# Kernel tuning notes

Measured on AMD Instinct MI355X. Metric: run time of the kernel, lower is better.

## Reference

```python
import jax, jax.numpy as jnp
import numpy as np

RADIUS = 0.5
K = 32
EPS = 1e-5


def ball_query(pc, new_pc, radius, k):
    """pc [B,3,N], new_pc [B,3,S] -> idx [B,S,k] int32, num [B,S] int32.
    First k in-radius points per query; empty slots filled with the first
    found index (standard ball-query semantics of QueryDepthPoint)."""
    d2 = jnp.sum((new_pc[:, :, :, None] - pc[:, :, None, :]) ** 2, axis=1)  # [B,S,N]
    B, S, N = d2.shape
    mask = d2 < radius * radius
    rank = jnp.cumsum(mask.astype(jnp.int32), axis=-1) - 1          # rank among valid
    slot = jnp.where(mask & (rank < k), rank, k)                     # k = dummy slot
    jidx = jnp.broadcast_to(jnp.arange(N, dtype=jnp.int32), (B, S, N))
    bidx = jnp.arange(B)[:, None, None]
    sidx = jnp.arange(S)[None, :, None]
    idx = jnp.zeros((B, S, k + 1), jnp.int32).at[bidx, sidx, slot].set(jidx)
    idx = idx[..., :k]
    num = jnp.sum(mask, axis=-1).astype(jnp.int32)                   # [B,S]
    nvalid = jnp.minimum(num, k)
    idx = jnp.where(jnp.arange(k) < nvalid[..., None], idx, idx[..., :1])
    return idx, num


def conv_bn_relu(x, w, b, g, be):
    """1x1 Conv2d + BatchNorm2d (batch stats, training mode) + ReLU.
    x [B,Cin,S,K], w [Cout,Cin]."""
    y = jnp.einsum('bcsk,oc->bosk', x, w) + b[None, :, None, None]
    mean = jnp.mean(y, axis=(0, 2, 3), keepdims=True)
    var = jnp.var(y, axis=(0, 2, 3), keepdims=True)
    y = (y - mean) * jax.lax.rsqrt(var + EPS) * g[None, :, None, None] + be[None, :, None, None]
    return jax.nn.relu(y)


def setup_inputs() -> dict:
    key = jax.random.key(0)
    ks = jax.random.split(key, 8)
    B, N, S, C = 4, 8192, 2048, 16
    mlp = [32, 32, 64]
    cin = C + 3  # use_xyz concat
    pc = jax.random.normal(ks[0], (B, 3, N), jnp.float32)
    feat = jax.random.normal(ks[1], (B, C, N), jnp.float32)
    new_pc = jax.random.normal(ks[2], (B, 3, S), jnp.float32)
    def kaiming(k, co, ci):
        return jax.random.normal(k, (co, ci), jnp.float32) * np.sqrt(2.0 / ci)
    w1 = kaiming(ks[3], mlp[0], cin)
    w2 = kaiming(ks[4], mlp[1], mlp[0])
    w3 = kaiming(ks[5], mlp[2], mlp[1])
    return {
        'pc': pc, 'feat': feat, 'new_pc': new_pc,
        'w1': w1, 'b1': jnp.zeros((mlp[0],)), 'g1': jnp.ones((mlp[0],)), 'be1': jnp.zeros((mlp[0],)),
        'w2': w2, 'b2': jnp.zeros((mlp[1],)), 'g2': jnp.ones((mlp[1],)), 'be2': jnp.zeros((mlp[1],)),
        'w3': w3, 'b3': jnp.zeros((mlp[2],)), 'g3': jnp.ones((mlp[2],)), 'be3': jnp.zeros((mlp[2],)),
    }


def reference(pc, feat, new_pc, w1, b1, g1, be1, w2, b2, g2, be2, w3, b3, g3, be3):
    B = pc.shape[0]
    S = new_pc.shape[2]
    idx, num = ball_query(pc, new_pc, RADIUS, K)          # [B,S,K], [B,S]
    bidx = jnp.arange(B)[:, None, None]
    # gather neighbors: fancy index -> [B,S,K,3] / [B,S,K,Cf], then to channel-first
    grouped_pc = pc[bidx, :, idx].transpose(0, 3, 1, 2)   # [B,3,S,K]
    grouped_pc = grouped_pc - new_pc[:, :, :, None]       # center on query
    grouped_feat = feat[bidx, :, idx].transpose(0, 3, 1, 2)  # [B,Cf,S,K]
    x = jnp.concatenate([grouped_pc, grouped_feat], axis=1)  # [B,Cf+3,S,K]
    x = conv_bn_relu(x, w1, b1, g1, be1)
    x = conv_bn_relu(x, w2, b2, g2, be2)
    x = conv_bn_relu(x, w3, b3, g3, be3)
    valid = (num > 0).astype(x.dtype)[:, None, :, None]   # [B,1,S,1]
    return x * valid
```

## Files before the change

### kernel.cpp

```cpp
#include <hip/hip_runtime.h>

#define BQ_RADIUS2 0.25f
#define KK 32
#define NB 4
#define NP 8192
#define NS 2048
#define C1 32
#define C2 32
#define C3 64
#define EPSBN 1e-5f
#define RTOT 65536
#define MTOT (NB*NS*KK)
#define NSLOT 32

#define OFF_G     0
#define OFF_IDX   655360
#define OFF_VALID 917504
#define OFF_P1    925696
#define OFF_P2    927744
#define OFF_P3    929792
#define OFF_PAR1  933888
#define OFF_PAR2  933952
#define OFF_PAR3  934016

__global__ __launch_bounds__(256) void k_pack(const float* __restrict__ pc,
                                              const float* __restrict__ feat,
                                              float* __restrict__ g,
                                              float* __restrict__ partials) {
  const int t = blockIdx.x * 256 + threadIdx.x;
  if (t < 8192) partials[t] = 0.f;
  const int b = t >> 13;
  const int j = t & (NP - 1);
  const float* pcb = pc + b * 3 * NP;
  float* gp = g + (size_t)t * 20;
  gp[0] = pcb[j];
  gp[1] = pcb[NP + j];
  gp[2] = pcb[2 * NP + j];
  const float* fb = feat + b * 16 * NP;
#pragma unroll
  for (int c = 0; c < 16; c++) gp[3 + c] = fb[c * NP + j];
  gp[19] = 0.f;
}

__global__ __launch_bounds__(256) void k_ballquery(const float* __restrict__ pc,
                                                   const float* __restrict__ newpc,
                                                   int* __restrict__ idx,
                                                   int* __restrict__ valid) {
  __shared__ int buf[4][KK];
  const int tid = threadIdx.x;
  const int w = tid >> 6, lane = tid & 63;
  const int gq = blockIdx.x * 4 + w;
  const int b = gq >> 11, s = gq & (NS - 1);
  const float* np0 = newpc + b * 3 * NS;
  const float qx = np0[s], qy = np0[NS + s], qz = np0[2 * NS + s];
  const float* px = pc + b * 3 * NP;
  const float* py = px + NP;
  const float* pz = px + 2 * NP;
  if (lane == 0) buf[w][0] = 0;
  int cnt = 0;
  for (int j0 = 0; j0 < NP; j0 += 256) {
    const int jb = j0 + lane * 4;
    const float4 vx = *(const float4*)(px + jb);
    const float4 vy = *(const float4*)(py + jb);
    const float4 vz = *(const float4*)(pz + jb);
    int mm = 0;
    {
      float dx = __fsub_rn(qx, vx.x), dy = __fsub_rn(qy, vy.x), dz = __fsub_rn(qz, vz.x);
      if (__fadd_rn(__fadd_rn(__fmul_rn(dx, dx), __fmul_rn(dy, dy)), __fmul_rn(dz, dz)) < BQ_RADIUS2) mm |= 1;
    }
    {
      float dx = __fsub_rn(qx, vx.y), dy = __fsub_rn(qy, vy.y), dz = __fsub_rn(qz, vz.y);
      if (__fadd_rn(__fadd_rn(__fmul_rn(dx, dx), __fmul_rn(dy, dy)), __fmul_rn(dz, dz)) < BQ_RADIUS2) mm |= 2;
    }
    {
      float dx = __fsub_rn(qx, vx.z), dy = __fsub_rn(qy, vy.z), dz = __fsub_rn(qz, vz.z);
      if (__fadd_rn(__fadd_rn(__fmul_rn(dx, dx), __fmul_rn(dy, dy)), __fmul_rn(dz, dz)) < BQ_RADIUS2) mm |= 4;
    }
    {
      float dx = __fsub_rn(qx, vx.w), dy = __fsub_rn(qy, vy.w), dz = __fsub_rn(qz, vz.w);
      if (__fadd_rn(__fadd_rn(__fmul_rn(dx, dx), __fmul_rn(dy, dy)), __fmul_rn(dz, dz)) < BQ_RADIUS2) mm |= 8;
    }
    const int c4 = __popc(mm);
    int pre = c4;
#pragma unroll
    for (int off = 1; off < 64; off <<= 1) {
      int v = __shfl_up(pre, off);
      if (lane >= off) pre += v;
    }
    const int total = __shfl(pre, 63);
    if (mm) {
      int base = cnt + pre - c4;
#pragma unroll
      for (int i = 0; i < 4; i++) {
        if ((mm >> i) & 1) {
          if (base < KK) buf[w][base] = jb + i;
          base++;
        }
      }
    }
    cnt += total;
    if (cnt >= KK) break;
  }
  __syncthreads();
  if (lane < KK) {
    const int f = cnt < KK ? cnt : KK;
    const int i0 = buf[w][0];
    idx[gq * KK + lane] = (lane < f) ? buf[w][lane] : i0;
  }
  if (lane == 0) valid[gq] = (cnt > 0);
}

__global__ __launch_bounds__(256, 1) void k_conv1(const float* __restrict__ g,
                                                  const int* __restrict__ idx,
                                                  const float* __restrict__ newpc,
                                                  const float* __restrict__ w1,
                                                  const float* __restrict__ b1,
                                                  float* __restrict__ y,
                                                  float* __restrict__ partial) {
  __shared__ float wl[C1 * 20];
  __shared__ float bl[C1];
  __shared__ float red[16][2 * C1 + 1];
  const int tid = threadIdx.x;
  for (int i = tid; i < C1 * 20; i += 256) {
    const int o = i / 20, c = i - o * 20;
    wl[i] = (c < 19) ? w1[o * 19 + c] : 0.f;
  }
  if (tid < C1) bl[tid] = b1[tid];
  __syncthreads();
  const int pos = blockIdx.x * 256 + tid;
  const int p4 = pos << 2;
  const int b = p4 >> 16;
  const int r = p4 & (RTOT - 1);
  const int s = r >> 5;
  const int4 jj = *(const int4*)(idx + p4);
  const float* np0 = newpc + b * 3 * NS;
  const float nx = np0[s], ny = np0[NS + s], nz = np0[2 * NS + s];
  float4 xr[20];
#define LOADPT(COMP, J) { \
    const float4* gp = (const float4*)(g + (size_t)(b * NP + (J)) * 20); \
    const float4 a0 = gp[0], a1 = gp[1], a2 = gp[2], a3 = gp[3], a4 = gp[4]; \
    xr[0].COMP = a0.x - nx; xr[1].COMP = a0.y - ny; xr[2].COMP = a0.z - nz; xr[3].COMP = a0.w; \
    xr[4].COMP = a1.x; xr[5].COMP = a1.y; xr[6].COMP = a1.z; xr[7].COMP = a1.w; \
    xr[8].COMP = a2.x; xr[9].COMP = a2.y; xr[10].COMP = a2.z; xr[11].COMP = a2.w; \
    xr[12].COMP = a3.x; xr[13].COMP = a3.y; xr[14].COMP = a3.z; xr[15].COMP = a3.w; \
    xr[16].COMP = a4.x; xr[17].COMP = a4.y; xr[18].COMP = a4.z; xr[19].COMP = a4.w; }
  LOADPT(x, jj.x) LOADPT(y, jj.y) LOADPT(z, jj.z) LOADPT(w, jj.w)
#undef LOADPT
  float* yb = y + ((size_t)b * C3) * RTOT + r;
  const int grp = tid >> 4;
  const bool lead = (tid & 15) == 0;
#pragma unroll 4
  for (int o = 0; o < C1; o++) {
    const float bo = bl[o];
    float4 acc = make_float4(bo, bo, bo, bo);
    const float4* wr = (const float4*)&wl[o * 20];
#pragma unroll
    for (int ct = 0; ct < 5; ct++) {
      const float4 wv = wr[ct];
      const float4 x0 = xr[4 * ct + 0], x1 = xr[4 * ct + 1], x2 = xr[4 * ct + 2], x3 = xr[4 * ct + 3];
      acc.x = fmaf(wv.x, x0.x, acc.x); acc.y = fmaf(wv.x, x0.y, acc.y);
      acc.z = fmaf(wv.x, x0.z, acc.z); acc.w = fmaf(wv.x, x0.w, acc.w);
      acc.x = fmaf(wv.y, x1.x, acc.x); acc.y = fmaf(wv.y, x1.y, acc.y);
      acc.z = fmaf(wv.y, x1.z, acc.z); acc.w = fmaf(wv.y, x1.w, acc.w);
      acc.x = fmaf(wv.z, x2.x, acc.x); acc.y = fmaf(wv.z, x2.y, acc.y);
      acc.z = fmaf(wv.z, x2.z, acc.z); acc.w = fmaf(wv.z, x2.w, acc.w);
      acc.x = fmaf(wv.w, x3.x, acc.x); acc.y = fmaf(wv.w, x3.y, acc.y);
      acc.z = fmaf(wv.w, x3.z, acc.z); acc.w = fmaf(wv.w, x3.w, acc.w);
    }
    *(float4*)(yb + (size_t)o * RTOT) = acc;
    float a = (acc.x + acc.y) + (acc.z + acc.w);
    float q = (acc.x * acc.x + acc.y * acc.y) + (acc.z * acc.z + acc.w * acc.w);
    a += __shfl_xor(a, 1); q += __shfl_xor(q, 1);
    a += __shfl_xor(a, 2); q += __shfl_xor(q, 2);
    a += __shfl_xor(a, 4); q += __shfl_xor(q, 4);
    a += __shfl_xor(a, 8); q += __shfl_xor(q, 8);
    if (lead) { red[grp][o] = a; red[grp][C1 + o] = q; }
  }
  __syncthreads();
  if (tid < 2 * C1) {
    float v = 0.f;
#pragma unroll
    for (int gq = 0; gq < 16; gq++) v += red[gq][tid];
    atomicAdd(&partial[(blockIdx.x & (NSLOT - 1)) * 2 * C1 + tid], v);
  }
}

__global__ __launch_bounds__(256, 1) void k_conv2(const float* __restrict__ w2,
                                                  const float* __restrict__ b2,
                                                  const float* __restrict__ par,
                                                  float* y,
                                                  float* __restrict__ partial) {
  __shared__ float wl[C2 * C1];
  __shared__ float bl[C2];
  __shared__ float pl[2 * C1];
  __shared__ float red[16][2 * C2 + 1];
  const int tid = threadIdx.x;
  for (int i = tid; i < C2 * C1; i += 256) wl[i] = w2[i];
  if (tid < C2) bl[tid] = b2[tid];
  if (tid < 2 * C1) pl[tid] = par[tid];
  __syncthreads();
  const int pos = blockIdx.x * 256 + tid;
  const int p4 = pos << 2;
  const int b = p4 >> 16;
  const int r = p4 & (RTOT - 1);
  float* yb = y + ((size_t)b * C3) * RTOT + r;
  float4 xr[C1];
#pragma unroll
  for (int c = 0; c < C1; c++) {
    float4 v = *(const float4*)(yb + (size_t)c * RTOT);
    const float sc = pl[c], sh = pl[C1 + c];
    v.x = fmaxf(fmaf(v.x, sc, sh), 0.f);
    v.y = fmaxf(fmaf(v.y, sc, sh), 0.f);
    v.z = fmaxf(fmaf(v.z, sc, sh), 0.f);
    v.w = fmaxf(fmaf(v.w, sc, sh), 0.f);
    xr[c] = v;
  }
  const int grp = tid >> 4;
  const bool lead = (tid & 15) == 0;
#pragma unroll 4
  for (int o = 0; o < C2; o++) {
    const float bo = bl[o];
    float4 acc = make_float4(bo, bo, bo, bo);
    const float4* wr = (const float4*)&wl[o * C1];
#pragma unroll
    for (int ct = 0; ct < C1 / 4; ct++) {
      const float4 wv = wr[ct];
      const float4 x0 = xr[4 * ct + 0], x1 = xr[4 * ct + 1], x2 = xr[4 * ct + 2], x3 = xr[4 * ct + 3];
      acc.x = fmaf(wv.x, x0.x, acc.x); acc.y = fmaf(wv.x, x0.y, acc.y);
      acc.z = fmaf(wv.x, x0.z, acc.z); acc.w = fmaf(wv.x, x0.w, acc.w);
      acc.x = fmaf(wv.y, x1.x, acc.x); acc.y = fmaf(wv.y, x1.y, acc.y);
      acc.z = fmaf(wv.y, x1.z, acc.z); acc.w = fmaf(wv.y, x1.w, acc.w);
      acc.x = fmaf(wv.z, x2.x, acc.x); acc.y = fmaf(wv.z, x2.y, acc.y);
      acc.z = fmaf(wv.z, x2.z, acc.z); acc.w = fmaf(wv.z, x2.w, acc.w);
      acc.x = fmaf(wv.w, x3.x, acc.x); acc.y = fmaf(wv.w, x3.y, acc.y);
      acc.z = fmaf(wv.w, x3.z, acc.z); acc.w = fmaf(wv.w, x3.w, acc.w);
    }
    *(float4*)(yb + (size_t)o * RTOT) = acc;
    float a = (acc.x + acc.y) + (acc.z + acc.w);
    float q = (acc.x * acc.x + acc.y * acc.y) + (acc.z * acc.z + acc.w * acc.w);
    a += __shfl_xor(a, 1); q += __shfl_xor(q, 1);
    a += __shfl_xor(a, 2); q += __shfl_xor(q, 2);
    a += __shfl_xor(a, 4); q += __shfl_xor(q, 4);
    a += __shfl_xor(a, 8); q += __shfl_xor(q, 8);
    if (lead) { red[grp][o] = a; red[grp][C2 + o] = q; }
  }
  __syncthreads();
  if (tid < 2 * C2) {
    float v = 0.f;
#pragma unroll
    for (int gq = 0; gq < 16; gq++) v += red[gq][tid];
    atomicAdd(&partial[(blockIdx.x & (NSLOT - 1)) * 2 * C2 + tid], v);
  }
}

__global__ __launch_bounds__(256, 1) void k_conv3(const float* __restrict__ w3,
                                                  const float* __restrict__ b3,
                                                  const float* __restrict__ par,
                                                  float* y,
                                                  float* __restrict__ partial) {
  __shared__ float wl[C3 * C2];
  __shared__ float bl[C3];
  __shared__ float pl[2 * C2];
  __shared__ float red[16][2 * C3 + 1];
  const int tid = threadIdx.x;
  for (int i = tid; i < C3 * C2; i += 256) wl[i] = w3[i];
  if (tid < C3) bl[tid] = b3[tid];
  if (tid < 2 * C2) pl[tid] = par[tid];
  __syncthreads();
  const int pos = blockIdx.x * 256 + tid;
  const int p4 = pos << 2;
  const int b = p4 >> 16;
  const int r = p4 & (RTOT - 1);
  float* yb = y + ((size_t)b * C3) * RTOT + r;
  float4 xr[C2];
#pragma unroll
  for (int c = 0; c < C2; c++) {
    float4 v = *(const float4*)(yb + (size_t)c * RTOT);
    const float sc = pl[c], sh = pl[C2 + c];
    v.x = fmaxf(fmaf(v.x, sc, sh), 0.f);
    v.y = fmaxf(fmaf(v.y, sc, sh), 0.f);
    v.z = fmaxf(fmaf(v.z, sc, sh), 0.f);
    v.w = fmaxf(fmaf(v.w, sc, sh), 0.f);
    xr[c] = v;
  }
  const int grp = tid >> 4;
  const bool lead = (tid & 15) == 0;
#pragma unroll 4
  for (int o = 0; o < C3; o++) {
    const float bo = bl[o];
    float4 acc = make_float4(bo, bo, bo, bo);
    const float4* wr = (const float4*)&wl[o * C2];
#pragma unroll
    for (int ct = 0; ct < C2 / 4; ct++) {
      const float4 wv = wr[ct];
      const float4 x0 = xr[4 * ct + 0], x1 = xr[4 * ct + 1], x2 = xr[4 * ct + 2], x3 = xr[4 * ct + 3];
      acc.x = fmaf(wv.x, x0.x, acc.x); acc.y = fmaf(wv.x, x0.y, acc.y);
      acc.z = fmaf(wv.x, x0.z, acc.z); acc.w = fmaf(wv.x, x0.w, acc.w);
      acc.x = fmaf(wv.y, x1.x, acc.x); acc.y = fmaf(wv.y, x1.y, acc.y);
      acc.z = fmaf(wv.y, x1.z, acc.z); acc.w = fmaf(wv.y, x1.w, acc.w);
      acc.x = fmaf(wv.z, x2.x, acc.x); acc.y = fmaf(wv.z, x2.y, acc.y);
      acc.z = fmaf(wv.z, x2.z, acc.z); acc.w = fmaf(wv.z, x2.w, acc.w);
      acc.x = fmaf(wv.w, x3.x, acc.x); acc.y = fmaf(wv.w, x3.y, acc.y);
      acc.z = fmaf(wv.w, x3.z, acc.z); acc.w = fmaf(wv.w, x3.w, acc.w);
    }
    *(float4*)(yb + (size_t)o * RTOT) = acc;
    float a = (acc.x + acc.y) + (acc.z + acc.w);
    float q = (acc.x * acc.x + acc.y * acc.y) + (acc.z * acc.z + acc.w * acc.w);
    a += __shfl_xor(a, 1); q += __shfl_xor(q, 1);
    a += __shfl_xor(a, 2); q += __shfl_xor(q, 2);
    a += __shfl_xor(a, 4); q += __shfl_xor(q, 4);
    a += __shfl_xor(a, 8); q += __shfl_xor(q, 8);
    if (lead) { red[grp][o] = a; red[grp][C3 + o] = q; }
  }
  __syncthreads();
  if (tid < 2 * C3) {
    float v = 0.f;
#pragma unroll
    for (int gq = 0; gq < 16; gq++) v += red[gq][tid];
    atomicAdd(&partial[(blockIdx.x & (NSLOT - 1)) * 2 * C3 + tid], v);
  }
}

__global__ void k_params(const float* __restrict__ partial,
                         const float* __restrict__ gamma,
                         const float* __restrict__ beta,
                         float* __restrict__ params, int C) {
  __shared__ float tot[2 * C3];
  const int t = threadIdx.x;
  float v = 0.f;
#pragma unroll 1
  for (int sl = 0; sl < NSLOT; ++sl) v += partial[sl * 2 * C + t];
  tot[t] = v;
  __syncthreads();
  if (t < C) {
    const float inv = 1.0f / (float)MTOT;
    const float mean = tot[t] * inv;
    const float ex2 = tot[C + t] * inv;
    const float var = ex2 - mean * mean;
    const float sc = gamma[t] * rsqrtf(var + EPSBN);
    params[t] = sc;
    params[C + t] = beta[t] - mean * sc;
  }
}

__global__ __launch_bounds__(256) void k_final(float* __restrict__ out,
                                               const float* __restrict__ par,
                                               const int* __restrict__ valid) {
  const int t = blockIdx.x * 256 + threadIdx.x;
  const size_t e = (size_t)t * 4;
  const int b = t >> 20;
  const int o = (t >> 14) & 63;
  const int s = (t & 16383) >> 3;
  const float sc = par[o], sh = par[C3 + o];
  const float m = valid[(b << 11) + s] ? 1.f : 0.f;
  float4 v = *(float4*)(out + e);
  v.x = fmaxf(fmaf(v.x, sc, sh), 0.f) * m;
  v.y = fmaxf(fmaf(v.y, sc, sh), 0.f) * m;
  v.z = fmaxf(fmaf(v.z, sc, sh), 0.f) * m;
  v.w = fmaxf(fmaf(v.w, sc, sh), 0.f) * m;
  *(float4*)(out + e) = v;
}

extern "C" void kernel_launch(void* const* d_in, const int* in_sizes, int n_in,
                              void* d_out, int out_size, void* d_ws, size_t ws_size,
                              hipStream_t stream) {
  const float* pc    = (const float*)d_in[0];
  const float* feat  = (const float*)d_in[1];
  const float* newpc = (const float*)d_in[2];
  const float* w1 = (const float*)d_in[3];
  const float* b1 = (const float*)d_in[4];
  const float* g1 = (const float*)d_in[5];
  const float* be1 = (const float*)d_in[6];
  const float* w2 = (const float*)d_in[7];
  const float* b2 = (const float*)d_in[8];
  const float* g2 = (const float*)d_in[9];
  const float* be2 = (const float*)d_in[10];
  const float* w3 = (const float*)d_in[11];
  const float* b3 = (const float*)d_in[12];
  const float* g3 = (const float*)d_in[13];
  const float* be3 = (const float*)d_in[14];

  float* ws = (float*)d_ws;
  float* gbuf  = ws + OFF_G;
  int*   idx   = (int*)(ws + OFF_IDX);
  int*   valid = (int*)(ws + OFF_VALID);
  float* p1 = ws + OFF_P1;
  float* p2 = ws + OFF_P2;
  float* p3 = ws + OFF_P3;
  float* par1 = ws + OFF_PAR1;
  float* par2 = ws + OFF_PAR2;
  float* par3 = ws + OFF_PAR3;
  float* out = (float*)d_out;

  k_pack<<<dim3(128), dim3(256), 0, stream>>>(pc, feat, gbuf, p1);
  k_ballquery<<<dim3(2048), dim3(256), 0, stream>>>(pc, newpc, idx, valid);
  k_conv1<<<dim3(256), dim3(256), 0, stream>>>(gbuf, idx, newpc, w1, b1, out, p1);
  k_params<<<dim3(1), dim3(2 * C1), 0, stream>>>(p1, g1, be1, par1, C1);
  k_conv2<<<dim3(256), dim3(256), 0, stream>>>(w2, b2, par1, out, p2);
  k_params<<<dim3(1), dim3(2 * C2), 0, stream>>>(p2, g2, be2, par2, C2);
  k_conv3<<<dim3(256), dim3(256), 0, stream>>>(w3, b3, par2, out, p3);
  k_params<<<dim3(1), dim3(2 * C3), 0, stream>>>(p3, g3, be3, par3, C3);
  k_final<<<dim3(16384), dim3(256), 0, stream>>>(out, par3, valid);
}
```

Before: 245.5 us.

## Fuse conv/BN stages into one cooperative kernel with grid syncs

Replaces the three conv kernels, three BN parameter kernels and the final activation pass with a single cooperative kernel. Each thread keeps one gathered position's activations in registers across all three layers and uses grid-wide syncs to finalize batch-norm statistics between layers. This removes the intermediate round trips of activations through global memory and most launch overhead. In exchange it needs 1024 co-resident blocks of 256 threads with large per-thread register arrays, which risks spills or launch failure; if the cooperative launch fails, it falls back to the old multi-kernel path.

```diff
diff --git a/kernel.cpp b/kernel.cpp
--- a/kernel.cpp
+++ b/kernel.cpp
@@ -1,4 +1,7 @@
 #include <hip/hip_runtime.h>
+#include <hip/hip_cooperative_groups.h>
+
+namespace cg = cooperative_groups;
 
 #define BQ_RADIUS2 0.25f
 #define KK 32
@@ -110,7 +113,181 @@
   if (lane == 0) valid[gq] = (cnt > 0);
 }
 
-__global__ __launch_bounds__(256, 1) void k_conv1(const float* __restrict__ g,
+#define STAT_O(CC, O, ACC) { \
+    float a_ = (ACC), q_ = (ACC) * (ACC); \
+    a_ += __shfl_xor(a_, 1); q_ += __shfl_xor(q_, 1); \
+    a_ += __shfl_xor(a_, 2); q_ += __shfl_xor(q_, 2); \
+    a_ += __shfl_xor(a_, 4); q_ += __shfl_xor(q_, 4); \
+    a_ += __shfl_xor(a_, 8); q_ += __shfl_xor(q_, 8); \
+    if (lead) { red[grp][(O)] = a_; red[grp][(CC) + (O)] = q_; } }
+
+__global__ __launch_bounds__(256, 4) void k_mega(
+    const float* __restrict__ g, const int* __restrict__ idx,
+    const float* __restrict__ newpc, const int* __restrict__ valid,
+    const float* __restrict__ w1, const float* __restrict__ b1,
+    const float* __restrict__ g1, const float* __restrict__ be1,
+    const float* __restrict__ w2, const float* __restrict__ b2,
+    const float* __restrict__ g2, const float* __restrict__ be2,
+    const float* __restrict__ w3, const float* __restrict__ b3,
+    const float* __restrict__ g3, const float* __restrict__ be3,
+    float* __restrict__ out,
+    float* __restrict__ p1, float* __restrict__ p2, float* __restrict__ p3) {
+  cg::grid_group gridg = cg::this_grid();
+  __shared__ float red[16][2 * C3 + 1];
+  __shared__ float pl[2 * C3];
+  const int tid = threadIdx.x;
+  const int pos = blockIdx.x * 256 + tid;
+  const int b = pos >> 16;
+  const int r = pos & (RTOT - 1);
+  const int s = r >> 5;
+  const int grp = tid >> 4;
+  const bool lead = (tid & 15) == 0;
+  const int slot = blockIdx.x & (NSLOT - 1);
+
+  const int j = idx[pos];
+  const float4* gp = (const float4*)(g + (size_t)(b * NP + j) * 20);
+  const float4 a0 = gp[0], a1 = gp[1], a2 = gp[2], a3 = gp[3], a4 = gp[4];
+  const float* np0 = newpc + b * 3 * NS;
+  float xr[20];
+  xr[0] = a0.x - np0[s]; xr[1] = a0.y - np0[NS + s]; xr[2] = a0.z - np0[2 * NS + s]; xr[3] = a0.w;
+  xr[4] = a1.x; xr[5] = a1.y; xr[6] = a1.z; xr[7] = a1.w;
+  xr[8] = a2.x; xr[9] = a2.y; xr[10] = a2.z; xr[11] = a2.w;
+  xr[12] = a3.x; xr[13] = a3.y; xr[14] = a3.z; xr[15] = a3.w;
+  xr[16] = a4.x; xr[17] = a4.y; xr[18] = a4.z; xr[19] = a4.w;
+  float y1[C1];
+#pragma unroll 4
+  for (int o = 0; o < C1; o++) {
+    float acc = b1[o];
+    const float* wr = w1 + o * 19;
+#pragma unroll
+    for (int c = 0; c < 19; c++) acc = fmaf(wr[c], xr[c], acc);
+    y1[o] = acc;
+    STAT_O(C1, o, acc)
+  }
+  __syncthreads();
+  if (tid < 2 * C1) {
+    float v = 0.f;
+#pragma unroll
+    for (int gq = 0; gq < 16; gq++) v += red[gq][tid];
+    atomicAdd(&p1[slot * 2 * C1 + tid], v);
+  }
+  gridg.sync();
+  if (tid < C1) {
+    float sm = 0.f, sq = 0.f;
+#pragma unroll 1
+    for (int sl = 0; sl < NSLOT; sl++) {
+      sm += p1[sl * 2 * C1 + tid];
+      sq += p1[sl * 2 * C1 + C1 + tid];
+    }
+    const float inv = 1.f / (float)MTOT;
+    const float mean = sm * inv;
+    const float var = sq * inv - mean * mean;
+    const float sc = g1[tid] * rsqrtf(var + EPSBN);
+    pl[tid] = sc;
+    pl[C1 + tid] = be1[tid] - mean * sc;
+  }
+  __syncthreads();
+
+  float y2[C2];
+  {
+    float xn[C1];
+#pragma unroll
+    for (int c = 0; c < C1; c++) xn[c] = fmaxf(fmaf(y1[c], pl[c], pl[C1 + c]), 0.f);
+#pragma unroll 4
+    for (int o = 0; o < C2; o++) {
+      float acc = b2[o];
+      const float4* wr = (const float4*)(w2 + o * C1);
+#pragma unroll
+      for (int ct = 0; ct < C1 / 4; ct++) {
+        const float4 wv = wr[ct];
+        acc = fmaf(wv.x, xn[4 * ct + 0], acc);
+        acc = fmaf(wv.y, xn[4 * ct + 1], acc);
+        acc = fmaf(wv.z, xn[4 * ct + 2], acc);
+        acc = fmaf(wv.w, xn[4 * ct + 3], acc);
+      }
+      y2[o] = acc;
+      STAT_O(C2, o, acc)
+    }
+  }
+  __syncthreads();
+  if (tid < 2 * C2) {
+    float v = 0.f;
+#pragma unroll
+    for (int gq = 0; gq < 16; gq++) v += red[gq][tid];
+    atomicAdd(&p2[slot * 2 * C2 + tid], v);
+  }
+  gridg.sync();
+  if (tid < C2) {
+    float sm = 0.f, sq = 0.f;
+#pragma unroll 1
+    for (int sl = 0; sl < NSLOT; sl++) {
+      sm += p2[sl * 2 * C2 + tid];
+      sq += p2[sl * 2 * C2 + C2 + tid];
+    }
+    const float inv = 1.f / (float)MTOT;
+    const float mean = sm * inv;
+    const float var = sq * inv - mean * mean;
+    const float sc = g2[tid] * rsqrtf(var + EPSBN);
+    pl[tid] = sc;
+    pl[C2 + tid] = be2[tid] - mean * sc;
+  }
+  __syncthreads();
+
+  float y3[C3];
+  {
+    float xn[C2];
+#pragma unroll
+    for (int c = 0; c < C2; c++) xn[c] = fmaxf(fmaf(y2[c], pl[c], pl[C2 + c]), 0.f);
+#pragma unroll 4
+    for (int o = 0; o < C3; o++) {
+      float acc = b3[o];
+      const float4* wr = (const float4*)(w3 + o * C2);
+#pragma unroll
+      for (int ct = 0; ct < C2 / 4; ct++) {
+        const float4 wv = wr[ct];
+        acc = fmaf(wv.x, xn[4 * ct + 0], acc);
+        acc = fmaf(wv.y, xn[4 * ct + 1], acc);
+        acc = fmaf(wv.z, xn[4 * ct + 2], acc);
+        acc = fmaf(wv.w, xn[4 * ct + 3], acc);
+      }
+      y3[o] = acc;
+      STAT_O(C3, o, acc)
+    }
+  }
+  __syncthreads();
+  if (tid < 2 * C3) {
+    float v = 0.f;
+#pragma unroll
+    for (int gq = 0; gq < 16; gq++) v += red[gq][tid];
+    atomicAdd(&p3[slot * 2 * C3 + tid], v);
+  }
+  gridg.sync();
+  if (tid < C3) {
+    float sm = 0.f, sq = 0.f;
+#pragma unroll 1
+    for (int sl = 0; sl < NSLOT; sl++) {
+      sm += p3[sl * 2 * C3 + tid];
+      sq += p3[sl * 2 * C3 + C3 + tid];
+    }
+    const float inv = 1.f / (float)MTOT;
+    const float mean = sm * inv;
+    const float var = sq * inv - mean * mean;
+    const float sc = g3[tid] * rsqrtf(var + EPSBN);
+    pl[tid] = sc;
+    pl[C3 + tid] = be3[tid] - mean * sc;
+  }
+  __syncthreads();
+
+  const float m = valid[(b << 11) + s] ? 1.f : 0.f;
+  float* ob = out + ((size_t)b * C3) * RTOT + r;
+#pragma unroll 8
+  for (int o = 0; o < C3; o++) {
+    ob[(size_t)o * RTOT] = fmaxf(fmaf(y3[o], pl[o], pl[C3 + o]), 0.f) * m;
+  }
+}
+
+
+__global__ __launch_bounds__(256, 1) void f_conv1(const float* __restrict__ g,
                                                   const int* __restrict__ idx,
                                                   const float* __restrict__ newpc,
                                                   const float* __restrict__ w1,
@@ -185,7 +362,7 @@
   }
 }
 
-__global__ __launch_bounds__(256, 1) void k_conv2(const float* __restrict__ w2,
+__global__ __launch_bounds__(256, 1) void f_conv2(const float* __restrict__ w2,
                                                   const float* __restrict__ b2,
                                                   const float* __restrict__ par,
                                                   float* y,
@@ -253,7 +430,7 @@
   }
 }
 
-__global__ __launch_bounds__(256, 1) void k_conv3(const float* __restrict__ w3,
+__global__ __launch_bounds__(256, 1) void f_conv3(const float* __restrict__ w3,
                                                   const float* __restrict__ b3,
                                                   const float* __restrict__ par,
                                                   float* y,
@@ -321,7 +498,7 @@
   }
 }
 
-__global__ void k_params(const float* __restrict__ partial,
+__global__ void f_params(const float* __restrict__ partial,
                          const float* __restrict__ gamma,
                          const float* __restrict__ beta,
                          float* __restrict__ params, int C) {
@@ -343,7 +520,7 @@
   }
 }
 
-__global__ __launch_bounds__(256) void k_final(float* __restrict__ out,
+__global__ __launch_bounds__(256) void f_final(float* __restrict__ out,
                                                const float* __restrict__ par,
                                                const int* __restrict__ valid) {
   const int t = blockIdx.x * 256 + threadIdx.x;
@@ -394,11 +571,24 @@
 
   k_pack<<<dim3(128), dim3(256), 0, stream>>>(pc, feat, gbuf, p1);
   k_ballquery<<<dim3(2048), dim3(256), 0, stream>>>(pc, newpc, idx, valid);
-  k_conv1<<<dim3(256), dim3(256), 0, stream>>>(gbuf, idx, newpc, w1, b1, out, p1);
-  k_params<<<dim3(1), dim3(2 * C1), 0, stream>>>(p1, g1, be1, par1, C1);
-  k_conv2<<<dim3(256), dim3(256), 0, stream>>>(w2, b2, par1, out, p2);
-  k_params<<<dim3(1), dim3(2 * C2), 0, stream>>>(p2, g2, be2, par2, C2);
-  k_conv3<<<dim3(256), dim3(256), 0, stream>>>(w3, b3, par2, out, p3);
-  k_params<<<dim3(1), dim3(2 * C3), 0, stream>>>(p3, g3, be3, par3, C3);
-  k_final<<<dim3(16384), dim3(256), 0, stream>>>(out, par3, valid);
-}
+
+  void* args[] = {
+    (void*)&gbuf, (void*)&idx, (void*)&newpc, (void*)&valid,
+    (void*)&w1, (void*)&b1, (void*)&g1, (void*)&be1,
+    (void*)&w2, (void*)&b2, (void*)&g2, (void*)&be2,
+    (void*)&w3, (void*)&b3, (void*)&g3, (void*)&be3,
+    (void*)&out, (void*)&p1, (void*)&p2, (void*)&p3,
+  };
+  hipError_t rc = hipLaunchCooperativeKernel((const void*)k_mega, dim3(1024),
+                                             dim3(256), args, 0, stream);
+  if (rc != hipSuccess) {
+    (void)hipGetLastError();
+    f_conv1<<<dim3(256), dim3(256), 0, stream>>>(gbuf, idx, newpc, w1, b1, out, p1);
+    f_params<<<dim3(1), dim3(2 * C1), 0, stream>>>(p1, g1, be1, par1, C1);
+    f_conv2<<<dim3(256), dim3(256), 0, stream>>>(w2, b2, par1, out, p2);
+    f_params<<<dim3(1), dim3(2 * C2), 0, stream>>>(p2, g2, be2, par2, C2);
+    f_conv3<<<dim3(256), dim3(256), 0, stream>>>(w3, b3, par2, out, p3);
+    f_params<<<dim3(1), dim3(2 * C3), 0, stream>>>(p3, g3, be3, par3, C3);
+    f_final<<<dim3(16384), dim3(256), 0, stream>>>(out, par3, valid);
+  }
+}
```

Result: slower. 542.7 us (+121.1%).
